# Optimization experiments

Hardware: AMD Instinct MI355X
Metric: run time of the kernel (lower is better)

The kernel has to match this reference:

```python
import jax, jax.numpy as jnp
import numpy as np

NUM_ITEMS = 100000
HIDDEN = 128
NNZ = 1600000


def setup_inputs() -> dict:
    key = jax.random.key(0)
    k1, k2, k3, k4, k5, k6 = jax.random.split(key, 6)
    item_embedding_table = jax.random.normal(k1, (NUM_ITEMS, HIDDEN), dtype=jnp.float32)
    adj_rows = jnp.sort(jax.random.randint(k2, (NNZ,), 0, NUM_ITEMS, dtype=jnp.int32))
    adj_cols = jax.random.randint(k3, (NNZ,), 0, NUM_ITEMS, dtype=jnp.int32)
    adj_vals = jax.random.uniform(k4, (NNZ,), dtype=jnp.float32)
    # nn.Linear default init (uniform in +-1/sqrt(fan_in)) approximated by scaled normal
    W_weight = jax.random.normal(k5, (HIDDEN, HIDDEN), dtype=jnp.float32) / np.sqrt(HIDDEN)
    W_bias = jax.random.normal(k6, (HIDDEN,), dtype=jnp.float32) * 0.01
    return {
        "item_embedding_table": item_embedding_table,
        "adj_rows": adj_rows,
        "adj_cols": adj_cols,
        "adj_vals": adj_vals,
        "W_weight": W_weight,
        "W_bias": W_bias,
    }


def reference(item_embedding_table, adj_rows, adj_cols, adj_vals, W_weight, W_bias):
    # support = W(x): x @ W^T + b   (nn.Linear convention: weight [out, in])
    support = jnp.einsum("nd,hd->nh", item_embedding_table, W_weight) + W_bias  # [N, H]
    # output = sparse_coo(adj) @ support, via gather + segment-sum scatter
    msgs = adj_vals[:, None] * support[adj_cols]  # [nnz, H]
    output = jax.ops.segment_sum(msgs, adj_rows, num_segments=NUM_ITEMS)  # [N, H]
    return output
```

## Files before the change

kernel.cpp:

```cpp
#include <hip/hip_runtime.h>
#include <hip/hip_fp16.h>

#define N_ITEMS 100000
#define HID 128
#define NNZ_T 1600000
#define RP_BLOCKS 391
#define GB_BLOCKS 1563
#define SPMM_BLOCKS 2048
#define WSTRIDE (SPMM_BLOCKS * 4)

typedef unsigned short ushort_t;
typedef unsigned int uint_t;
typedef short bf16x8 __attribute__((ext_vector_type(8)));
typedef float f32x4 __attribute__((ext_vector_type(4)));

static __device__ __forceinline__ ushort_t f32_to_bf16(float f) {
    uint_t u = __float_as_uint(f);
    uint_t r = (u + 0x7FFFu + ((u >> 16) & 1u)) >> 16;
    return (ushort_t)r;
}

__global__ __launch_bounds__(256) void prep_gemm(
    const float* __restrict__ X, const float* __restrict__ W,
    const float* __restrict__ bias, const int* __restrict__ rows,
    ushort_t* __restrict__ S, int* __restrict__ row_ptr) {
    if (blockIdx.x < RP_BLOCKS) {
        int r = blockIdx.x * 256 + threadIdx.x;
        if (r > N_ITEMS) return;
        int lo = 0, hi = NNZ_T;
        while (lo < hi) {
            int mid = (lo + hi) >> 1;
            if (rows[mid] < r) lo = mid + 1; else hi = mid;
        }
        row_ptr[r] = lo;
        return;
    }

    __shared__ ushort_t Wl[HID * HID];
    {
        const int t = threadIdx.x;
        const float4* Wf = (const float4*)W;
#pragma unroll
        for (int j = 0; j < 8; ++j) {
            const int gblk = j * 256 + t;
            float4 w0 = Wf[gblk * 2];
            float4 w1 = Wf[gblk * 2 + 1];
            bf16x8 v;
            v[0] = (short)f32_to_bf16(w0.x); v[1] = (short)f32_to_bf16(w0.y);
            v[2] = (short)f32_to_bf16(w0.z); v[3] = (short)f32_to_bf16(w0.w);
            v[4] = (short)f32_to_bf16(w1.x); v[5] = (short)f32_to_bf16(w1.y);
            v[6] = (short)f32_to_bf16(w1.z); v[7] = (short)f32_to_bf16(w1.w);
            const int ps = (gblk * 8) ^ (((gblk >> 4) & 7) << 3);
            *(bf16x8*)&Wl[ps] = v;
        }
    }
    __syncthreads();

    const int lane = threadIdx.x & 63;
    const int wave = threadIdx.x >> 6;
    const int m = lane & 15;
    const int q = lane >> 4;
    const int row0 = (blockIdx.x - RP_BLOCKS) * 64 + wave * 16;

    int arow = row0 + m;
    if (arow >= N_ITEMS) arow = N_ITEMS - 1;

    const int swz = (m & 7) << 3;
    f32x4 acc[8] = {};

#pragma unroll
    for (int kb = 0; kb < 4; ++kb) {
        const int k0 = kb * 32 + q * 8;
        float4 a0 = *(const float4*)&X[(size_t)arow * HID + k0];
        float4 a1 = *(const float4*)&X[(size_t)arow * HID + k0 + 4];
        bf16x8 xf;
        xf[0] = (short)f32_to_bf16(a0.x); xf[1] = (short)f32_to_bf16(a0.y);
        xf[2] = (short)f32_to_bf16(a0.z); xf[3] = (short)f32_to_bf16(a0.w);
        xf[4] = (short)f32_to_bf16(a1.x); xf[5] = (short)f32_to_bf16(a1.y);
        xf[6] = (short)f32_to_bf16(a1.z); xf[7] = (short)f32_to_bf16(a1.w);
#pragma unroll
        for (int nt = 0; nt < 8; ++nt) {
            const bf16x8 wf = *(const bf16x8*)&Wl[((nt * 16 + m) * HID + k0) ^ swz];
            acc[nt] = __builtin_amdgcn_mfma_f32_16x16x32_bf16(wf, xf, acc[nt], 0, 0, 0);
        }
    }

    const int srow = row0 + m;
    const bool ok = srow < N_ITEMS;
#pragma unroll
    for (int nt = 0; nt < 8; ++nt) {
        const int c0 = nt * 16 + q * 4;
        float4 bv = *(const float4*)&bias[c0];
        ushort_t h0 = __half_as_ushort(__float2half(acc[nt][0] + bv.x));
        ushort_t h1 = __half_as_ushort(__float2half(acc[nt][1] + bv.y));
        ushort_t h2 = __half_as_ushort(__float2half(acc[nt][2] + bv.z));
        ushort_t h3 = __half_as_ushort(__float2half(acc[nt][3] + bv.w));
        uint2 pk;
        pk.x = (uint_t)h0 | ((uint_t)h1 << 16);
        pk.y = (uint_t)h2 | ((uint_t)h3 << 16);
        if (ok) *(uint2*)&S[(size_t)srow * HID + c0] = pk;
    }
}

__global__ __launch_bounds__(256) void spmm_csr(
    const int* __restrict__ cols, const float* __restrict__ vals,
    const int* __restrict__ row_ptr, const ushort_t* __restrict__ S,
    float* __restrict__ out) {
    const int lane = threadIdx.x & 63;
    const int g = lane >> 4;
    const int l = lane & 15;
    const int sel = lane >> 5;
    const int NP = N_ITEMS / 2;

    int wid = blockIdx.x * 4 + (threadIdx.x >> 6);
    if (wid >= NP) return;
    int2 p01 = *(const int2*)&row_ptr[wid * 2];
    int pE2 = row_ptr[wid * 2 + 2];

    for (;;) {
        const int nwid = wid + WSTRIDE;
        const bool has_next = (nwid < NP);
        int2 np01 = p01; int npE2 = pE2;
        if (has_next) {
            np01 = *(const int2*)&row_ptr[nwid * 2];
            npE2 = row_ptr[nwid * 2 + 2];
        }

        int pa = p01.x; const int pEa = p01.y;
        int pb = p01.y; const int pEb = pE2;

        __half2 accA[4], accB[4];
#pragma unroll
        for (int j = 0; j < 4; ++j) { accA[j] = __float2half2_rn(0.f); accB[j] = __float2half2_rn(0.f); }

        if (pa < pEa || pb < pEb) {
            const int base = sel ? pb : pa;
            const int end  = sel ? pEb : pEa;
            const int idx  = base + l;
            const int cidx = max(min(idx, end - 1), 0);
            int   c_l = cols[cidx];
            float v_l = (idx < end) ? vals[cidx] : 0.f;

            for (;;) {
                const int pa2 = min(pa + 16, pEa);
                const int pb2 = min(pb + 16, pEb);
                const bool more = (pa2 < pEa) || (pb2 < pEb);
                int c_n = 0; float v_n = 0.f;
                if (more) {
                    const int b2 = sel ? pb2 : pa2;
                    const int e2 = sel ? pEb : pEa;
                    const int i2 = b2 + l;
                    const int ci2 = max(min(i2, e2 - 1), 0);
                    c_n = cols[ci2];
                    v_n = (i2 < e2) ? vals[ci2] : 0.f;
                }

                uint4 uA[4], uB[4];
                float vA[4], vB[4];
#pragma unroll
                for (int t = 0; t < 4; ++t) {
                    const int sa = 4 * t + g;
                    const int ca = __shfl(c_l, sa, 64);
                    vA[t] = __shfl(v_l, sa, 64);
                    uA[t] = *(const uint4*)&S[(size_t)ca * HID + 8 * l];
                    const int cb = __shfl(c_l, 32 + sa, 64);
                    vB[t] = __shfl(v_l, 32 + sa, 64);
                    uB[t] = *(const uint4*)&S[(size_t)cb * HID + 8 * l];
                }
#pragma unroll
                for (int t = 0; t < 4; ++t) {
                    const __half2 wa = __float2half2_rn(vA[t]);
                    accA[0] = __hfma2(wa, *(const __half2*)&uA[t].x, accA[0]);
                    accA[1] = __hfma2(wa, *(const __half2*)&uA[t].y, accA[1]);
                    accA[2] = __hfma2(wa, *(const __half2*)&uA[t].z, accA[2]);
                    accA[3] = __hfma2(wa, *(const __half2*)&uA[t].w, accA[3]);
                    const __half2 wb = __float2half2_rn(vB[t]);
                    accB[0] = __hfma2(wb, *(const __half2*)&uB[t].x, accB[0]);
                    accB[1] = __hfma2(wb, *(const __half2*)&uB[t].y, accB[1]);
                    accB[2] = __hfma2(wb, *(const __half2*)&uB[t].z, accB[2]);
                    accB[3] = __hfma2(wb, *(const __half2*)&uB[t].w, accB[3]);
                }
                if (!more) break;
                pa = pa2; pb = pb2; c_l = c_n; v_l = v_n;
            }
        }

        float fA[8], fB[8];
#pragma unroll
        for (int j = 0; j < 4; ++j) {
            fA[2 * j] = __low2float(accA[j]);  fA[2 * j + 1] = __high2float(accA[j]);
            fB[2 * j] = __low2float(accB[j]);  fB[2 * j + 1] = __high2float(accB[j]);
        }
#pragma unroll
        for (int e = 0; e < 8; ++e) {
            fA[e] += __shfl_xor(fA[e], 16, 64);
            fA[e] += __shfl_xor(fA[e], 32, 64);
            fB[e] += __shfl_xor(fB[e], 16, 64);
            fB[e] += __shfl_xor(fB[e], 32, 64);
        }
        const int r0 = wid * 2;
        if (g == 0) {
            float* p = &out[(size_t)r0 * HID + 8 * l];
            *(float4*)p       = make_float4(fA[0], fA[1], fA[2], fA[3]);
            *(float4*)(p + 4) = make_float4(fA[4], fA[5], fA[6], fA[7]);
        } else if (g == 1 && r0 + 1 < N_ITEMS) {
            float* p = &out[(size_t)(r0 + 1) * HID + 8 * l];
            *(float4*)p       = make_float4(fB[0], fB[1], fB[2], fB[3]);
            *(float4*)(p + 4) = make_float4(fB[4], fB[5], fB[6], fB[7]);
        }

        if (!has_next) break;
        wid = nwid; p01 = np01; pE2 = npE2;
    }
}

extern "C" void kernel_launch(void* const* d_in, const int* in_sizes, int n_in,
                              void* d_out, int out_size, void* d_ws, size_t ws_size,
                              hipStream_t stream) {
    const float* X    = (const float*)d_in[0];
    const int*   rows = (const int*)  d_in[1];
    const int*   cols = (const int*)  d_in[2];
    const float* vals = (const float*)d_in[3];
    const float* W    = (const float*)d_in[4];
    const float* bias = (const float*)d_in[5];
    float* out = (float*)d_out;

    ushort_t* S       = (ushort_t*)d_ws;
    int*      row_ptr = (int*)(S + (size_t)N_ITEMS * HID);

    prep_gemm<<<RP_BLOCKS + GB_BLOCKS, 256, 0, stream>>>(X, W, bias, rows, S, row_ptr);
    spmm_csr<<<SPMM_BLOCKS, 256, 0, stream>>>(cols, vals, row_ptr, S, out);
}
```

Before: 188.5 us.

## Process four rows per wave with merged nnz stream and fp32 dot2 accumulation

The SpMM kernel is restructured so each wave handles four consecutive rows as one contiguous nnz range, consuming 32 nonzeros per iteration. Each nonzero is routed to the right row accumulator by segment boundaries, with a masked path for groups that straddle a boundary. Accumulation switches from half2 FMA to fp32 via the fdot2 builtin. The grid-stride loop and row_ptr prefetch are replaced by a one-shot launch of 6250 blocks. This is meant to cut per-row loop overhead and the idle lanes on short rows, and to improve accuracy, at the cost of more registers and branchy accumulator selection.

```diff
diff --git a/kernel.cpp b/kernel.cpp
--- a/kernel.cpp
+++ b/kernel.cpp
@@ -6,19 +6,37 @@
 #define NNZ_T 1600000
 #define RP_BLOCKS 391
 #define GB_BLOCKS 1563
-#define SPMM_BLOCKS 2048
-#define WSTRIDE (SPMM_BLOCKS * 4)
+#define SPMM_BLOCKS 6250
 
 typedef unsigned short ushort_t;
 typedef unsigned int uint_t;
 typedef short bf16x8 __attribute__((ext_vector_type(8)));
 typedef float f32x4 __attribute__((ext_vector_type(4)));
+typedef _Float16 h2_t __attribute__((ext_vector_type(2)));
 
 static __device__ __forceinline__ ushort_t f32_to_bf16(float f) {
     uint_t u = __float_as_uint(f);
     uint_t r = (u + 0x7FFFu + ((u >> 16) & 1u)) >> 16;
     return (ushort_t)r;
 }
+
+static __device__ __forceinline__ float fdot2w(uint_t w, uint_t h, float acc) {
+#if __has_builtin(__builtin_amdgcn_fdot2)
+    return __builtin_amdgcn_fdot2(__builtin_bit_cast(h2_t, w),
+                                  __builtin_bit_cast(h2_t, h), acc, false);
+#else
+    __half2 hv = *(__half2*)&h; __half2 wv = *(__half2*)&w;
+    return acc + __low2float(wv) * __low2float(hv)
+               + __high2float(wv) * __high2float(hv);
+#endif
+}
+
+#define DOT8(A, U, WLO, WHI) do {                                       \
+    A[0] = fdot2w(WLO, (U).x, A[0]); A[1] = fdot2w(WHI, (U).x, A[1]);   \
+    A[2] = fdot2w(WLO, (U).y, A[2]); A[3] = fdot2w(WHI, (U).y, A[3]);   \
+    A[4] = fdot2w(WLO, (U).z, A[4]); A[5] = fdot2w(WHI, (U).z, A[5]);   \
+    A[6] = fdot2w(WLO, (U).w, A[6]); A[7] = fdot2w(WHI, (U).w, A[7]);   \
+} while (0)
 
 __global__ __launch_bounds__(256) void prep_gemm(
     const float* __restrict__ X, const float* __restrict__ W,
@@ -109,108 +127,83 @@
     const int lane = threadIdx.x & 63;
     const int g = lane >> 4;
     const int l = lane & 15;
-    const int sel = lane >> 5;
-    const int NP = N_ITEMS / 2;
-
-    int wid = blockIdx.x * 4 + (threadIdx.x >> 6);
-    if (wid >= NP) return;
-    int2 p01 = *(const int2*)&row_ptr[wid * 2];
-    int pE2 = row_ptr[wid * 2 + 2];
-
-    for (;;) {
-        const int nwid = wid + WSTRIDE;
-        const bool has_next = (nwid < NP);
-        int2 np01 = p01; int npE2 = pE2;
-        if (has_next) {
-            np01 = *(const int2*)&row_ptr[nwid * 2];
-            npE2 = row_ptr[nwid * 2 + 2];
-        }
-
-        int pa = p01.x; const int pEa = p01.y;
-        int pb = p01.y; const int pEb = pE2;
-
-        __half2 accA[4], accB[4];
-#pragma unroll
-        for (int j = 0; j < 4; ++j) { accA[j] = __float2half2_rn(0.f); accB[j] = __float2half2_rn(0.f); }
-
-        if (pa < pEa || pb < pEb) {
-            const int base = sel ? pb : pa;
-            const int end  = sel ? pEb : pEa;
-            const int idx  = base + l;
-            const int cidx = max(min(idx, end - 1), 0);
-            int   c_l = cols[cidx];
-            float v_l = (idx < end) ? vals[cidx] : 0.f;
-
-            for (;;) {
-                const int pa2 = min(pa + 16, pEa);
-                const int pb2 = min(pb + 16, pEb);
-                const bool more = (pa2 < pEa) || (pb2 < pEb);
-                int c_n = 0; float v_n = 0.f;
-                if (more) {
-                    const int b2 = sel ? pb2 : pa2;
-                    const int e2 = sel ? pEb : pEa;
-                    const int i2 = b2 + l;
-                    const int ci2 = max(min(i2, e2 - 1), 0);
-                    c_n = cols[ci2];
-                    v_n = (i2 < e2) ? vals[ci2] : 0.f;
-                }
-
-                uint4 uA[4], uB[4];
-                float vA[4], vB[4];
-#pragma unroll
-                for (int t = 0; t < 4; ++t) {
-                    const int sa = 4 * t + g;
-                    const int ca = __shfl(c_l, sa, 64);
-                    vA[t] = __shfl(v_l, sa, 64);
-                    uA[t] = *(const uint4*)&S[(size_t)ca * HID + 8 * l];
-                    const int cb = __shfl(c_l, 32 + sa, 64);
-                    vB[t] = __shfl(v_l, 32 + sa, 64);
-                    uB[t] = *(const uint4*)&S[(size_t)cb * HID + 8 * l];
-                }
-#pragma unroll
-                for (int t = 0; t < 4; ++t) {
-                    const __half2 wa = __float2half2_rn(vA[t]);
-                    accA[0] = __hfma2(wa, *(const __half2*)&uA[t].x, accA[0]);
-                    accA[1] = __hfma2(wa, *(const __half2*)&uA[t].y, accA[1]);
-                    accA[2] = __hfma2(wa, *(const __half2*)&uA[t].z, accA[2]);
-                    accA[3] = __hfma2(wa, *(const __half2*)&uA[t].w, accA[3]);
-                    const __half2 wb = __float2half2_rn(vB[t]);
-                    accB[0] = __hfma2(wb, *(const __half2*)&uB[t].x, accB[0]);
-                    accB[1] = __hfma2(wb, *(const __half2*)&uB[t].y, accB[1]);
-                    accB[2] = __hfma2(wb, *(const __half2*)&uB[t].z, accB[2]);
-                    accB[3] = __hfma2(wb, *(const __half2*)&uB[t].w, accB[3]);
-                }
-                if (!more) break;
-                pa = pa2; pb = pb2; c_l = c_n; v_l = v_n;
+    const int wid = blockIdx.x * 4 + (threadIdx.x >> 6);
+    const int r0 = wid * 4;
+    if (r0 >= N_ITEMS) return;
+
+    const int4 p = *(const int4*)&row_ptr[r0];
+    const int pend = row_ptr[r0 + 4];
+    const int b1 = p.y, b2 = p.z, b3 = p.w;
+
+    float a0[8] = {}, a1x[8] = {}, a2x[8] = {}, a3[8] = {};
+
+    for (int base = p.x; base < pend; base += 32) {
+        const int idx = base + (lane & 31);
+        const int cidx = min(idx, pend - 1);
+        const int c_l = cols[cidx];
+        const float v_l = (idx < pend) ? vals[cidx] : 0.f;
+
+        int ct[8]; float vt[8];
+#pragma unroll
+        for (int t = 0; t < 8; ++t) {
+            ct[t] = __shfl(c_l, 4 * t + g, 64);
+            vt[t] = __shfl(v_l, 4 * t + g, 64);
+        }
+        uint4 u[8];
+#pragma unroll
+        for (int t = 0; t < 8; ++t)
+            u[t] = *(const uint4*)&S[(size_t)ct[t] * HID + 8 * l];
+
+#pragma unroll
+        for (int t = 0; t < 8; ++t) {
+            const int s_lo = base + 4 * t;
+            const int s_hi = s_lo + 3;
+            if (s_lo >= pend) continue;
+            const uint_t vh = (uint_t)__half_as_ushort(__float2half(vt[t]));
+            const uint_t wlo = vh;
+            const uint_t whi = vh << 16;
+            if (s_lo >= b3)                   { DOT8(a3, u[t], wlo, whi); }
+            else if (s_hi < b1)               { DOT8(a0, u[t], wlo, whi); }
+            else if (s_lo >= b1 && s_hi < b2) { DOT8(a1x, u[t], wlo, whi); }
+            else if (s_lo >= b2 && s_hi < b3) { DOT8(a2x, u[t], wlo, whi); }
+            else {
+                const int s = s_lo + g;
+                const bool c0 = (s < b1);
+                const bool c1 = (s >= b1) && (s < b2);
+                const bool c2 = (s >= b2) && (s < b3);
+                const bool c3 = (s >= b3);
+                const uint_t w0l = c0 ? wlo : 0u, w0h = c0 ? whi : 0u;
+                const uint_t w1l = c1 ? wlo : 0u, w1h = c1 ? whi : 0u;
+                const uint_t w2l = c2 ? wlo : 0u, w2h = c2 ? whi : 0u;
+                const uint_t w3l = c3 ? wlo : 0u, w3h = c3 ? whi : 0u;
+                DOT8(a0, u[t], w0l, w0h);
+                DOT8(a1x, u[t], w1l, w1h);
+                DOT8(a2x, u[t], w2l, w2h);
+                DOT8(a3, u[t], w3l, w3h);
             }
         }
-
-        float fA[8], fB[8];
-#pragma unroll
-        for (int j = 0; j < 4; ++j) {
-            fA[2 * j] = __low2float(accA[j]);  fA[2 * j + 1] = __high2float(accA[j]);
-            fB[2 * j] = __low2float(accB[j]);  fB[2 * j + 1] = __high2float(accB[j]);
-        }
-#pragma unroll
-        for (int e = 0; e < 8; ++e) {
-            fA[e] += __shfl_xor(fA[e], 16, 64);
-            fA[e] += __shfl_xor(fA[e], 32, 64);
-            fB[e] += __shfl_xor(fB[e], 16, 64);
-            fB[e] += __shfl_xor(fB[e], 32, 64);
-        }
-        const int r0 = wid * 2;
-        if (g == 0) {
-            float* p = &out[(size_t)r0 * HID + 8 * l];
-            *(float4*)p       = make_float4(fA[0], fA[1], fA[2], fA[3]);
-            *(float4*)(p + 4) = make_float4(fA[4], fA[5], fA[6], fA[7]);
-        } else if (g == 1 && r0 + 1 < N_ITEMS) {
-            float* p = &out[(size_t)(r0 + 1) * HID + 8 * l];
-            *(float4*)p       = make_float4(fB[0], fB[1], fB[2], fB[3]);
-            *(float4*)(p + 4) = make_float4(fB[4], fB[5], fB[6], fB[7]);
-        }
-
-        if (!has_next) break;
-        wid = nwid; p01 = np01; pE2 = npE2;
+    }
+
+#pragma unroll
+    for (int e = 0; e < 8; ++e) {
+        a0[e] += __shfl_xor(a0[e], 16, 64);  a0[e] += __shfl_xor(a0[e], 32, 64);
+        a1x[e] += __shfl_xor(a1x[e], 16, 64); a1x[e] += __shfl_xor(a1x[e], 32, 64);
+        a2x[e] += __shfl_xor(a2x[e], 16, 64); a2x[e] += __shfl_xor(a2x[e], 32, 64);
+        a3[e] += __shfl_xor(a3[e], 16, 64);  a3[e] += __shfl_xor(a3[e], 32, 64);
+    }
+    float* po = &out[(size_t)(r0 + g) * HID + 8 * l];
+    if (g == 0) {
+        *(float4*)po       = make_float4(a0[0], a0[1], a0[2], a0[3]);
+        *(float4*)(po + 4) = make_float4(a0[4], a0[5], a0[6], a0[7]);
+    } else if (g == 1) {
+        *(float4*)po       = make_float4(a1x[0], a1x[1], a1x[2], a1x[3]);
+        *(float4*)(po + 4) = make_float4(a1x[4], a1x[5], a1x[6], a1x[7]);
+    } else if (g == 2) {
+        *(float4*)po       = make_float4(a2x[0], a2x[1], a2x[2], a2x[3]);
+        *(float4*)(po + 4) = make_float4(a2x[4], a2x[5], a2x[6], a2x[7]);
+    } else {
+        *(float4*)po       = make_float4(a3[0], a3[1], a3[2], a3[3]);
+        *(float4*)(po + 4) = make_float4(a3[4], a3[5], a3[6], a3[7]);
     }
 }
 
```

New measurement: 189.9 us. Within noise of the previous version (+0.7%).
